# Kernel optimization log

Hardware: AMD Instinct MI355X
Metric: run time of the kernel (lower is better)

The kernel has to match this reference:

```python
import jax, jax.numpy as jnp
import numpy as np

HEADS, K = 8, 32
EPS = 1e-5


def bn(x, gamma, beta):
    # batch-stat BN over all axes except the last (channel) axis
    axes = tuple(range(x.ndim - 1))
    m = jnp.mean(x, axes, keepdims=True)
    v = jnp.var(x, axes, keepdims=True)
    return (x - m) / jnp.sqrt(v + EPS) * gamma + beta


def leaky(z):
    return jax.nn.leaky_relu(z, 0.2)


def conv1(t, W, g, b):  # 1x1 Conv1d + BN + LeakyReLU, channels-last
    return leaky(bn(jnp.einsum('bnc,dc->bnd', t, W), g, b))


def conv2(t, W, g, b):  # 1x1 Conv2d + BN + LeakyReLU on (B,N,k,C)
    return leaky(bn(jnp.einsum('bnkc,dc->bnkd', t, W), g, b))


def _forward(x, pos, Wq, gq, bq, Wk, gk, bk, Wv, gv, bv,
             Wpb, gpb, bpb, We1, ge1, be1, We2, ge2, be2,
             Wm1, gm1, bm1, Wm2, gm2, bm2):
    B, N, C = x.shape
    cph = C // HEADS
    q = conv1(x, Wq, gq, bq)
    key = conv1(x, Wk, gk, bk)
    val = conv1(x, Wv, gv, bv)
    # kNN in key-feature space (DGCNN-style get_graph_feature, edge_function='global')
    sq = jnp.sum(key * key, -1)                          # (B,N)
    dist = sq[:, :, None] + sq[:, None, :] - 2.0 * jnp.einsum('bnc,bmc->bnm', key, key)
    _, idx = jax.lax.top_k(-dist, K)                     # (B,N,K)
    bidx = jnp.arange(B)[:, None, None]
    key_nb = key[bidx, idx]                              # (B,N,K,C)
    val_nb = val[bidx, idx]
    pos_nb = pos[bidx, idx]
    mask = jnp.sign(idx + 1).astype(x.dtype)             # (B,N,K), all ones for valid knn
    masked_pos = (pos_nb - pos[:, :, None, :]) * mask[..., None]
    posb = conv2(masked_pos, Wpb, gpb, bpb)              # (B,N,K,C)
    vector = key_nb - q[:, :, None, :] + posb            # vector attention logits input
    value = val_nb + posb
    vector = conv2(conv2(vector, We1, ge1, be1), We2, ge2, be2)  # (B,N,K,cph)
    vector = jax.nn.softmax(vector, axis=2) * mask[..., None]    # softmax over k neighbors
    value = value.reshape(B, N, K, cph, HEADS)
    attn = jnp.einsum('bnkgh,bnkg->bngh', value, vector).reshape(B, N, C)
    x = x + attn
    h = jax.nn.silu(bn(jnp.einsum('bnc,dc->bnd', x, Wm1), gm1, bm1))
    m = jax.nn.silu(bn(jnp.einsum('bnc,dc->bnd', h, Wm2), gm2, bm2))
    return x + m


def setup_inputs():
    key = jax.random.key(0)
    ks = jax.random.split(key, 16)
    B, N, C, H = 2, 2048, 256, 512
    cph = C // HEADS
    s = 0.02
    inp = {
        'x': jax.random.normal(ks[0], (B, N, C), jnp.float32),
        'pos': jax.random.normal(ks[1], (B, N, C), jnp.float32),
        'Wq': jax.random.normal(ks[2], (C, C), jnp.float32) * s,
        'gq': jnp.ones((C,), jnp.float32), 'bq': jnp.zeros((C,), jnp.float32),
        'Wk': jax.random.normal(ks[3], (C, C), jnp.float32) * s,
        'gk': jnp.ones((C,), jnp.float32), 'bk': jnp.zeros((C,), jnp.float32),
        'Wv': jax.random.normal(ks[4], (C, C), jnp.float32) * s,
        'gv': jnp.ones((C,), jnp.float32), 'bv': jnp.zeros((C,), jnp.float32),
        'Wpb': jax.random.normal(ks[5], (C, C), jnp.float32) * s,
        'gpb': jnp.ones((C,), jnp.float32), 'bpb': jnp.zeros((C,), jnp.float32),
        'We1': jax.random.normal(ks[6], (cph, C), jnp.float32) * s,
        'ge1': jnp.ones((cph,), jnp.float32), 'be1': jnp.zeros((cph,), jnp.float32),
        'We2': jax.random.normal(ks[7], (cph, cph), jnp.float32) * s,
        'ge2': jnp.ones((cph,), jnp.float32), 'be2': jnp.zeros((cph,), jnp.float32),
        'Wm1': jax.random.normal(ks[8], (H, C), jnp.float32) * s,
        'gm1': jnp.ones((H,), jnp.float32), 'bm1': jnp.zeros((H,), jnp.float32),
        'Wm2': jax.random.normal(ks[9], (C, H), jnp.float32) * s,
        'gm2': jnp.ones((C,), jnp.float32), 'bm2': jnp.zeros((C,), jnp.float32),
    }
    return inp


def reference(x, pos, Wq, gq, bq, Wk, gk, bk, Wv, gv, bv,
              Wpb, gpb, bpb, We1, ge1, be1, We2, ge2, be2,
              Wm1, gm1, bm1, Wm2, gm2, bm2):
    return _forward(x, pos, Wq, gq, bq, Wk, gk, bk, Wv, gv, bv,
                    Wpb, gpb, bpb, We1, ge1, be1, We2, ge2, be2,
                    Wm1, gm1, bm1, Wm2, gm2, bm2)
```

## Files before the change

### kernel.cpp

```cpp
#include <hip/hip_runtime.h>

#define EPS 1e-5f

typedef __attribute__((ext_vector_type(8))) short s8v;
typedef __attribute__((ext_vector_type(4))) float f4v;

__device__ __forceinline__ float leakyf(float z){ return z >= 0.f ? z : 0.2f*z; }
__device__ __forceinline__ float siluf(float y){ return y / (1.f + __expf(-y)); }
__device__ __forceinline__ unsigned f2bfu(float f){
  unsigned u = __float_as_uint(f);
  return (u + 0x7FFFu + ((u>>16)&1u)) >> 16;
}
__device__ __forceinline__ unsigned short bfr(float f){ return (unsigned short)f2bfu(f); }
__device__ __forceinline__ float bf2f16(unsigned short s){ return __uint_as_float(((unsigned)s)<<16); }

__global__ __launch_bounds__(256) void k_zero(float* __restrict__ p, int n){
  int i = blockIdx.x*256 + threadIdx.x;
  if (i < n) p[i] = 0.f;
}

template<bool TRANSA, bool STATS, bool FULL4>
__global__ __launch_bounds__(256) void k_gemm(
    const float* __restrict__ A, int lda, long aStr,
    const float* __restrict__ A3, int lda3,
    const float* __restrict__ fAbuck, float invnA, int CA,
    const float* __restrict__ gA, const float* __restrict__ bA,
    const float* __restrict__ B0, const float* __restrict__ B1,
    const float* __restrict__ B2, const float* __restrict__ B3, int ldb, long bStr,
    float* __restrict__ C, int ldc, long cStr,
    float* __restrict__ C3, int ldc3,
    int K, float* __restrict__ buck, int statC, int statChanStr)
{
  __shared__ unsigned short Ah[2048], Al[2048], Bh[2048], Bl[2048];
  __shared__ float Ssum[STATS?64:4], Ssq[STATS?64:4];
  __shared__ float mrA[TRANSA?1024:4];
  const int z = blockIdx.z;
  const bool zAlt = (A3 != nullptr) && (z == 3);
  const float* Az = zAlt ? A3 : A + (long)z*aStr;
  const int ldaz = zAlt ? lda3 : lda;
  const float* Bb = (z==0?B0 : z==1?B1 : (z==2?B2:B3)) + (long)z*bStr;
  float* Cb = zAlt ? C3 : (C + (long)z*cStr);
  const int ldcz = zAlt ? ldc3 : ldc;
  const bool doStats = STATS && !zAlt;
  const int tid = threadIdx.x;
  const int bm = blockIdx.x*64, bn = blockIdx.y*64;
  const int wv = tid>>6, lane = tid&63;
  const int lm = lane&15, quad = lane>>4;
  if (doStats && tid<64){ Ssum[tid]=0.f; Ssq[tid]=0.f; }
  if (TRANSA){
    for (int c = tid; c < CA; c += 256){
      float s=0.f, q=0.f;
      for (int b=0;b<64;b++){ s += fAbuck[(long)b*2*CA + c]; q += fAbuck[(long)b*2*CA + CA + c]; }
      float m = s*invnA;
      float v = fmaxf(q*invnA - m*m, 0.f);
      mrA[c] = m; mrA[CA + c] = rsqrtf(v + EPS);
    }
    __syncthreads();
  }

  const int r0 = tid>>3, kg = tid&7;
  const int qk = kg>>1, j0 = (kg&1)*4;
  const int s0 = ((((r0>>4)  )*4 + qk)*16 + ((r0&15)^qk))*8 + j0;
  const int s1 = ((((r0>>4)+2)*4 + qk)*16 + ((r0&15)^qk))*8 + j0;
  const float* aP0 = Az + (long)(bm+r0)*ldaz + kg*4;
  const float* aP1 = aP0 + (long)32*ldaz;
  const float* bP0 = Bb + (long)(bn+r0)*ldb + kg*4;
  const float* bP1 = bP0 + (long)32*ldb;

  f4v acc[4];
  #pragma unroll
  for (int j=0;j<4;j++) acc[j] = (f4v){0.f,0.f,0.f,0.f};

  float4 a0 = *(const float4*)(aP0);
  float4 a1 = *(const float4*)(aP1);
  float4 b0 = *(const float4*)(bP0);
  float4 b1 = *(const float4*)(bP1);

  for (int k0=0; k0<K; k0+=32){
    float4 av0 = a0, av1 = a1;
    if (TRANSA){
      float4 m4 = *(const float4*)&mrA[k0 + kg*4];
      float4 r4 = *(const float4*)&mrA[CA + k0 + kg*4];
      float4 g4 = *(const float4*)(gA + k0 + kg*4);
      float4 b4 = *(const float4*)(bA + k0 + kg*4);
      av0.x = siluf((av0.x - m4.x)*r4.x*g4.x + b4.x);
      av0.y = siluf((av0.y - m4.y)*r4.y*g4.y + b4.y);
      av0.z = siluf((av0.z - m4.z)*r4.z*g4.z + b4.z);
      av0.w = siluf((av0.w - m4.w)*r4.w*g4.w + b4.w);
      av1.x = siluf((av1.x - m4.x)*r4.x*g4.x + b4.x);
      av1.y = siluf((av1.y - m4.y)*r4.y*g4.y + b4.y);
      av1.z = siluf((av1.z - m4.z)*r4.z*g4.z + b4.z);
      av1.w = siluf((av1.w - m4.w)*r4.w*g4.w + b4.w);
    }
    ushort4 h4, l4;
    h4.x=bfr(av0.x); l4.x=bfr(av0.x-bf2f16(h4.x));
    h4.y=bfr(av0.y); l4.y=bfr(av0.y-bf2f16(h4.y));
    h4.z=bfr(av0.z); l4.z=bfr(av0.z-bf2f16(h4.z));
    h4.w=bfr(av0.w); l4.w=bfr(av0.w-bf2f16(h4.w));
    *(ushort4*)&Ah[s0]=h4; *(ushort4*)&Al[s0]=l4;
    h4.x=bfr(av1.x); l4.x=bfr(av1.x-bf2f16(h4.x));
    h4.y=bfr(av1.y); l4.y=bfr(av1.y-bf2f16(h4.y));
    h4.z=bfr(av1.z); l4.z=bfr(av1.z-bf2f16(h4.z));
    h4.w=bfr(av1.w); l4.w=bfr(av1.w-bf2f16(h4.w));
    *(ushort4*)&Ah[s1]=h4; *(ushort4*)&Al[s1]=l4;
    h4.x=bfr(b0.x); l4.x=bfr(b0.x-bf2f16(h4.x));
    h4.y=bfr(b0.y); l4.y=bfr(b0.y-bf2f16(h4.y));
    h4.z=bfr(b0.z); l4.z=bfr(b0.z-bf2f16(h4.z));
    h4.w=bfr(b0.w); l4.w=bfr(b0.w-bf2f16(h4.w));
    *(ushort4*)&Bh[s0]=h4; *(ushort4*)&Bl[s0]=l4;
    h4.x=bfr(b1.x); l4.x=bfr(b1.x-bf2f16(h4.x));
    h4.y=bfr(b1.y); l4.y=bfr(b1.y-bf2f16(h4.y));
    h4.z=bfr(b1.z); l4.z=bfr(b1.z-bf2f16(h4.z));
    h4.w=bfr(b1.w); l4.w=bfr(b1.w-bf2f16(h4.w));
    *(ushort4*)&Bh[s1]=h4; *(ushort4*)&Bl[s1]=l4;
    __syncthreads();
    if (k0+32 < K){
      a0 = *(const float4*)(aP0 + k0+32);
      a1 = *(const float4*)(aP1 + k0+32);
      b0 = *(const float4*)(bP0 + k0+32);
      b1 = *(const float4*)(bP1 + k0+32);
    }
    const int soA = ((wv*4 + quad)*16 + (lm^quad))*8;
    s8v ah = *(const s8v*)&Ah[soA];
    s8v al = *(const s8v*)&Al[soA];
    #pragma unroll
    for (int j=0;j<4;j++){
      const int soB = ((j*4 + quad)*16 + (lm^quad))*8;
      s8v bh = *(const s8v*)&Bh[soB];
      s8v bl = *(const s8v*)&Bl[soB];
      acc[j] = __builtin_amdgcn_mfma_f32_16x16x32_bf16(ah, bh, acc[j], 0,0,0);
      acc[j] = __builtin_amdgcn_mfma_f32_16x16x32_bf16(ah, bl, acc[j], 0,0,0);
      acc[j] = __builtin_amdgcn_mfma_f32_16x16x32_bf16(al, bh, acc[j], 0,0,0);
      if (FULL4)
        acc[j] = __builtin_amdgcn_mfma_f32_16x16x32_bf16(al, bl, acc[j], 0,0,0);
    }
    __syncthreads();
  }
  #pragma unroll
  for (int rr=0;rr<4;rr++){
    float* cr = Cb + (long)(bm + wv*16 + quad*4 + rr)*ldcz + bn + lm;
    #pragma unroll
    for (int j=0;j<4;j++) cr[j*16] = acc[j][rr];
  }
  if (doStats){
    #pragma unroll
    for (int j=0;j<4;j++){
      float s=0.f, q=0.f;
      #pragma unroll
      for (int rr=0;rr<4;rr++){ float v = acc[j][rr]; s += v; q += v*v; }
      s += __shfl_xor(s,16,64); s += __shfl_xor(s,32,64);
      q += __shfl_xor(q,16,64); q += __shfl_xor(q,32,64);
      if (quad==0){ atomicAdd(&Ssum[j*16+lm], s); atomicAdd(&Ssq[j*16+lm], q); }
    }
    __syncthreads();
    if (tid < 64){
      int chan = statChanStr*z + bn + tid;
      float* bb = buck + (long)(blockIdx.x & 63)*2*statC;
      atomicAdd(&bb[chan], Ssum[tid]);
      atomicAdd(&bb[statC + chan], Ssq[tid]);
    }
  }
}

__global__ void k_finalize(const float* __restrict__ buck, int C, float invn, float* __restrict__ mr){
  int c = blockIdx.x*256 + threadIdx.x;
  if (c < C){
    float s=0,q=0;
    for (int b=0;b<64;b++){ s += buck[(long)b*2*C + c]; q += buck[(long)b*2*C + C + c]; }
    float m = s*invn;
    float v = fmaxf(q*invn - m*m, 0.f);
    mr[c] = m; mr[C+c] = rsqrtf(v + EPS);
  }
}

__global__ __launch_bounds__(256) void k_apply_qkv(const float* __restrict__ raw, const float* __restrict__ bQKV,
    const float* __restrict__ gq, const float* __restrict__ bq,
    const float* __restrict__ gk, const float* __restrict__ bk,
    const float* __restrict__ gv, const float* __restrict__ bv,
    float* __restrict__ key, float* __restrict__ qv, float* __restrict__ sq){
  __shared__ float mrs[1536];
  __shared__ float red[4];
  const int tid = threadIdx.x;
  const int wv = tid>>6, lane = tid&63;
  for (int c = tid; c < 768; c += 256){
    float s=0.f, q=0.f;
    for (int b=0;b<64;b++){ s += bQKV[(long)b*1536 + c]; q += bQKV[(long)b*1536 + 768 + c]; }
    float m = s*(1.f/4096.f);
    float v = fmaxf(q*(1.f/4096.f) - m*m, 0.f);
    mrs[c] = m; mrs[768+c] = rsqrtf(v + EPS);
  }
  __syncthreads();
  const float gqv = gq[tid], bqv = bq[tid], gkv = gk[tid], bkv = bk[tid], gvv = gv[tid], bvv = bv[tid];
  for (int rr=0; rr<8; rr++){
    const long r = (long)blockIdx.x*8 + rr;
    const float* row = raw + r*768;
    float zq = row[tid], zk = row[256+tid], zv = row[512+tid];
    float yq = leakyf((zq - mrs[tid])*mrs[768+tid]*gqv + bqv);
    float yk = leakyf((zk - mrs[256+tid])*mrs[1024+tid]*gkv + bkv);
    float yv = leakyf((zv - mrs[512+tid])*mrs[1280+tid]*gvv + bvv);
    qv[r*512 + tid] = yq;
    key[r*256 + tid] = yk;
    qv[r*512 + 256 + tid] = yv;
    float kq = yk*yk;
    kq += __shfl_xor(kq,1,64); kq += __shfl_xor(kq,2,64);
    kq += __shfl_xor(kq,4,64); kq += __shfl_xor(kq,8,64);
    kq += __shfl_xor(kq,16,64); kq += __shfl_xor(kq,32,64);
    if (lane==0) red[wv] = kq;
    __syncthreads();
    if (tid==0) sq[r] = red[0]+red[1]+red[2]+red[3];
    __syncthreads();
  }
}

__global__ __launch_bounds__(256) void k_topk(const float* __restrict__ G2, const float* __restrict__ sq,
    int* __restrict__ idxb, const float* __restrict__ P, float* __restrict__ bPB){
  __shared__ unsigned Ds[4][2048];
  __shared__ int Ws[4][32];
  const int wv = threadIdx.x >> 6, lane = threadIdx.x & 63;
  const int row = blockIdx.x*4 + wv;
  const int b = row >> 11, n = row & 2047;
  const float* Grow = G2 + (long)b*4194304 + (long)n*2048;
  const float* sqb = sq + b*2048;
  const float sqn = sqb[n];
  const unsigned long long SEN = 0xFFFFFFFFFFFFFFFFull;
  unsigned long long k0=SEN,k1=SEN,k2=SEN,k3=SEN;
  #pragma unroll
  for (int j=0;j<32;j++){
    int m = lane + j*64;
    float d = sqn + sqb[m] - 2.f*Grow[m];
    unsigned u = __float_as_uint(d);
    u ^= ((unsigned)((int)u >> 31)) | 0x80000000u;
    Ds[wv][m] = u;
    unsigned long long kk = ((unsigned long long)u << 32) | (unsigned)m;
    if (kk < k3){
      k3 = kk;
      if (k3 < k2){ unsigned long long t_=k2; k2=k3; k3=t_; }
      if (k2 < k1){ unsigned long long t_=k1; k1=k2; k2=t_; }
      if (k1 < k0){ unsigned long long t_=k0; k0=k1; k1=t_; }
    }
  }
  int* orow = idxb + row*32;
  for (int t=0;t<32;t++){
    unsigned long long v = k0;
    #pragma unroll
    for (int off=32; off; off>>=1){
      unsigned long long v2 = (unsigned long long)__shfl_xor((long long)v, off, 64);
      if (v2 < v) v = v2;
    }
    int wi = (int)(v & 0xFFFFFFFFull);
    if (lane == 0){ orow[t] = wi; Ws[wv][t] = wi; }
    if (v == k0){
      Ds[wv][wi] = 0xFFFFFFFFu;
      k0=k1; k1=k2; k2=k3; k3=SEN;
      if (k0 == SEN){
        for (int j=0;j<32;j++){
          int m = lane + j*64;
          unsigned u = Ds[wv][m];
          if (u != 0xFFFFFFFFu){
            unsigned long long kk = ((unsigned long long)u << 32) | (unsigned)m;
            if (kk < k3){
              k3 = kk;
              if (k3 < k2){ unsigned long long t_=k2; k2=k3; k3=t_; }
              if (k2 < k1){ unsigned long long t_=k1; k1=k2; k2=t_; }
              if (k1 < k0){ unsigned long long t_=k0; k0=k1; k1=t_; }
            }
          }
        }
      }
    }
  }
  const long bbase = (long)b << 11;
  const int c4 = lane*4;
  float4 pn = *(const float4*)(P + (long)row*256 + c4);
  float s0=0,s1=0,s2=0,s3=0,q0=0,q1=0,q2=0,q3=0;
  #pragma unroll
  for (int t=0;t<32;t++){
    float4 pg = *(const float4*)(P + (bbase + Ws[wv][t])*256 + c4);
    float z0 = pg.x - pn.x, z1 = pg.y - pn.y, z2 = pg.z - pn.z, z3 = pg.w - pn.w;
    s0+=z0; q0+=z0*z0; s1+=z1; q1+=z1*z1;
    s2+=z2; q2+=z2*z2; s3+=z3; q3+=z3*z3;
  }
  float* bb = bPB + (long)(blockIdx.x & 63)*512;
  atomicAdd(&bb[c4+0], s0); atomicAdd(&bb[c4+1], s1);
  atomicAdd(&bb[c4+2], s2); atomicAdd(&bb[c4+3], s3);
  atomicAdd(&bb[256+c4+0], q0); atomicAdd(&bb[256+c4+1], q1);
  atomicAdd(&bb[256+c4+2], q2); atomicAdd(&bb[256+c4+3], q3);
}

__global__ __launch_bounds__(256) void k_e1m(
    const float* __restrict__ key, const float* __restrict__ qv, const float* __restrict__ P,
    const int* __restrict__ idx, const float* __restrict__ mrPB,
    const float* __restrict__ gpb, const float* __restrict__ bpb,
    const float* __restrict__ We1, float* __restrict__ E1, float* __restrict__ buckE1)
{
  __shared__ unsigned short Ab[16384];
  __shared__ unsigned short Wb[8192];
  __shared__ float Ssum[32], Ssq[32];
  const int tid = threadIdx.x;
  const int wv = tid>>6, lane = tid&63;
  const int quad = lane>>4, lm = lane&15;
  const int bn0 = blockIdx.x*2;
  if (tid < 32){ Ssum[tid]=0.f; Ssq[tid]=0.f; }
  for (int e = tid; e < 8192; e += 256){
    int d = e >> 8, c = e & 255;
    int off = (((d>>4)*8 + (c>>5))*4 + ((c>>3)&3))*128 + (d&15)*8 + (c&7);
    Wb[off] = bfr(We1[e]);
  }
  {
    const int bn = bn0 + (wv>>1);
    const long base = (long)(bn >> 11) << 11;
    const int c4 = lane*4;
    float4 q4  = *(const float4*)(qv + (long)bn*512 + c4);
    float4 pn4 = *(const float4*)(P + (long)bn*256 + c4);
    float4 mp4 = *(const float4*)(mrPB + c4);
    float4 rp4 = *(const float4*)(mrPB + 256 + c4);
    float4 g4  = *(const float4*)(gpb + c4);
    float4 b4  = *(const float4*)(bpb + c4);
    const int ksc = c4>>5, quadc = (c4>>3)&3, jc = c4&7;
    for (int j = 0; j < 16; ++j){
      const int rloc = wv*16 + j;
      const int kk = rloc & 31;
      const int g = idx[bn*32 + kk];
      float4 kb = *(const float4*)(key + (base+g)*256 + c4);
      float4 pb = *(const float4*)(P + (base+g)*256 + c4);
      float o0 = kb.x - q4.x + leakyf((pb.x - pn4.x - mp4.x)*rp4.x*g4.x + b4.x);
      float o1 = kb.y - q4.y + leakyf((pb.y - pn4.y - mp4.y)*rp4.y*g4.y + b4.y);
      float o2 = kb.z - q4.z + leakyf((pb.z - pn4.z - mp4.z)*rp4.z*g4.z + b4.z);
      float o3 = kb.w - q4.w + leakyf((pb.w - pn4.w - mp4.w)*rp4.w*g4.w + b4.w);
      const int atile = rloc >> 4;
      const int slot = ((rloc & 15) ^ (ksc<<1) ^ quadc) & 15;
      const int off = ((atile*8 + ksc)*4 + quadc)*128 + slot*8 + jc;
      ushort4 u; u.x = bfr(o0); u.y = bfr(o1); u.z = bfr(o2); u.w = bfr(o3);
      *(ushort4*)&Ab[off] = u;
    }
  }
  __syncthreads();
  f4v acc0 = (f4v){0,0,0,0}, acc1 = (f4v){0,0,0,0};
  #pragma unroll
  for (int ks=0; ks<8; ks++){
    const int aslot = (lm ^ (ks<<1) ^ quad) & 15;
    s8v a  = *(const s8v*)&Ab[((wv*8 + ks)*4 + quad)*128 + aslot*8];
    s8v b0 = *(const s8v*)&Wb[((ks)*4 + quad)*128 + lm*8];
    s8v b1 = *(const s8v*)&Wb[((8 + ks)*4 + quad)*128 + lm*8];
    acc0 = __builtin_amdgcn_mfma_f32_16x16x32_bf16(a, b0, acc0, 0,0,0);
    acc1 = __builtin_amdgcn_mfma_f32_16x16x32_bf16(a, b1, acc1, 0,0,0);
  }
  {
    const int bn = bn0 + (wv>>1);
    const int mt = wv & 1;
    #pragma unroll
    for (int rr=0; rr<4; rr++){
      int krow = mt*16 + quad*4 + rr;
      float* o = E1 + ((long)bn*32 + krow)*32;
      o[lm]      = acc0[rr];
      o[16 + lm] = acc1[rr];
    }
  }
  float s0=0,q0=0,s1=0,q1=0;
  #pragma unroll
  for (int rr=0; rr<4; rr++){
    s0 += acc0[rr]; q0 += acc0[rr]*acc0[rr];
    s1 += acc1[rr]; q1 += acc1[rr]*acc1[rr];
  }
  s0 += __shfl_xor(s0,16,64); s0 += __shfl_xor(s0,32,64);
  q0 += __shfl_xor(q0,16,64); q0 += __shfl_xor(q0,32,64);
  s1 += __shfl_xor(s1,16,64); s1 += __shfl_xor(s1,32,64);
  q1 += __shfl_xor(q1,16,64); q1 += __shfl_xor(q1,32,64);
  if (quad == 0){
    atomicAdd(&Ssum[lm], s0);      atomicAdd(&Ssq[lm], q0);
    atomicAdd(&Ssum[16+lm], s1);   atomicAdd(&Ssq[16+lm], q1);
  }
  __syncthreads();
  if (tid < 32){
    float* bb = buckE1 + (long)(blockIdx.x & 63)*64;
    atomicAdd(&bb[tid], Ssum[tid]); atomicAdd(&bb[32+tid], Ssq[tid]);
  }
}

__global__ __launch_bounds__(256) void k_e2m(
    float* __restrict__ E, const float* __restrict__ bE1buck,
    const float* __restrict__ ge1, const float* __restrict__ be1,
    const float* __restrict__ We2, float* __restrict__ buckE2)
{
  __shared__ unsigned short Ab[8192];
  __shared__ unsigned short Wb[1024];
  __shared__ float Ssum[32], Ssq[32];
  __shared__ float mrE1s[64];
  const int tid = threadIdx.x;
  const int wv = tid>>6, lane = tid&63;
  const int quad = lane>>4, lm = lane&15;
  const long r0 = (long)blockIdx.x*256;
  if (tid < 32){
    Ssum[tid]=0.f; Ssq[tid]=0.f;
    float s=0.f, q=0.f;
    for (int b=0;b<64;b++){ s += bE1buck[b*64+tid]; q += bE1buck[b*64+32+tid]; }
    float m = s*(1.f/131072.f);
    float v = fmaxf(q*(1.f/131072.f) - m*m, 0.f);
    mrE1s[tid] = m; mrE1s[32+tid] = rsqrtf(v + EPS);
  }
  for (int e = tid; e < 1024; e += 256){
    int d = e>>5, c = e&31;
    int off = ((d>>4)*4 + ((c>>3)&3))*128 + (d&15)*8 + (c&7);
    Wb[off] = bfr(We2[e]);
  }
  __syncthreads();
  #pragma unroll
  for (int it=0; it<8; it++){
    int e = (tid + it*256)*4;
    int row = e>>5, c = e&31;
    float4 v = *(const float4*)(E + (r0 + row)*32 + c);
    float4 m4 = *(const float4*)&mrE1s[c];
    float4 r4 = *(const float4*)&mrE1s[32+c];
    float4 g4 = *(const float4*)(ge1 + c);
    float4 b4 = *(const float4*)(be1 + c);
    float o0 = leakyf((v.x - m4.x)*r4.x*g4.x + b4.x);
    float o1 = leakyf((v.y - m4.y)*r4.y*g4.y + b4.y);
    float o2 = leakyf((v.z - m4.z)*r4.z*g4.z + b4.z);
    float o3 = leakyf((v.w - m4.w)*r4.w*g4.w + b4.w);
    int quadc = (c>>3)&3, jc = c&7;
    int slot = ((row&15) ^ quadc) & 15;
    int off = ((row>>4)*4 + quadc)*128 + slot*8 + jc;
    ushort4 u; u.x=bfr(o0); u.y=bfr(o1); u.z=bfr(o2); u.w=bfr(o3);
    *(ushort4*)&Ab[off] = u;
  }
  __syncthreads();
  f4v acc0[4], acc1[4];
  #pragma unroll
  for (int i=0;i<4;i++){ acc0[i]=(f4v){0,0,0,0}; acc1[i]=(f4v){0,0,0,0}; }
  const int aslot = (lm ^ quad) & 15;
  s8v b0 = *(const s8v*)&Wb[(quad)*128 + lm*8];
  s8v b1 = *(const s8v*)&Wb[(4 + quad)*128 + lm*8];
  #pragma unroll
  for (int i=0;i<4;i++){
    const int atile = wv*4 + i;
    s8v a = *(const s8v*)&Ab[(atile*4 + quad)*128 + aslot*8];
    acc0[i] = __builtin_amdgcn_mfma_f32_16x16x32_bf16(a, b0, acc0[i], 0,0,0);
    acc1[i] = __builtin_amdgcn_mfma_f32_16x16x32_bf16(a, b1, acc1[i], 0,0,0);
  }
  __syncthreads();
  float s0=0,q0=0,s1=0,q1=0;
  #pragma unroll
  for (int i=0;i<4;i++){
    const int atile = wv*4 + i;
    #pragma unroll
    for (int rr=0; rr<4; rr++){
      long row = r0 + atile*16 + quad*4 + rr;
      float* o = E + row*32;
      o[lm]      = acc0[i][rr];
      o[16 + lm] = acc1[i][rr];
      s0 += acc0[i][rr]; q0 += acc0[i][rr]*acc0[i][rr];
      s1 += acc1[i][rr]; q1 += acc1[i][rr]*acc1[i][rr];
    }
  }
  s0 += __shfl_xor(s0,16,64); s0 += __shfl_xor(s0,32,64);
  q0 += __shfl_xor(q0,16,64); q0 += __shfl_xor(q0,32,64);
  s1 += __shfl_xor(s1,16,64); s1 += __shfl_xor(s1,32,64);
  q1 += __shfl_xor(q1,16,64); q1 += __shfl_xor(q1,32,64);
  if (quad == 0){
    atomicAdd(&Ssum[lm], s0);    atomicAdd(&Ssq[lm], q0);
    atomicAdd(&Ssum[16+lm], s1); atomicAdd(&Ssq[16+lm], q1);
  }
  __syncthreads();
  if (tid < 32){
    float* bb = buckE2 + (long)(blockIdx.x & 63)*64;
    atomicAdd(&bb[tid], Ssum[tid]); atomicAdd(&bb[32+tid], Ssq[tid]);
  }
}

__global__ __launch_bounds__(256) void k_attn(
    const float* __restrict__ E2, const float* __restrict__ bE2buck,
    const float* __restrict__ ge2, const float* __restrict__ be2,
    const float* __restrict__ qv, const float* __restrict__ P, const int* __restrict__ idx,
    const float* __restrict__ mrPB, const float* __restrict__ gpb, const float* __restrict__ bpb,
    const float* __restrict__ xin, float* __restrict__ x2)
{
  __shared__ float L[4][32][33];
  __shared__ float mrE2s[64];
  const int tid = threadIdx.x;
  const int wv = tid>>6, lane = tid&63;
  if (tid < 32){
    float s=0.f, q=0.f;
    for (int b=0;b<64;b++){ s += bE2buck[b*64+tid]; q += bE2buck[b*64+32+tid]; }
    float m = s*(1.f/131072.f);
    float v = fmaxf(q*(1.f/131072.f) - m*m, 0.f);
    mrE2s[tid] = m; mrE2s[32+tid] = rsqrtf(v + EPS);
  }
  __syncthreads();
  const int bn = blockIdx.x*4 + wv;
  const long base = (long)(bn >> 11) << 11;
  for (int qq=0; qq<4; qq++){
    int e = lane*16 + qq*4;
    int k = e >> 5, g0 = e & 31;
    float4 v  = *(const float4*)(E2 + (long)bn*1024 + e);
    float4 m4 = *(const float4*)&mrE2s[g0];
    float4 r4 = *(const float4*)&mrE2s[32+g0];
    float4 g4 = *(const float4*)(ge2 + g0);
    float4 b4 = *(const float4*)(be2 + g0);
    L[wv][k][g0+0] = leakyf((v.x - m4.x)*r4.x*g4.x + b4.x);
    L[wv][k][g0+1] = leakyf((v.y - m4.y)*r4.y*g4.y + b4.y);
    L[wv][k][g0+2] = leakyf((v.z - m4.z)*r4.z*g4.z + b4.z);
    L[wv][k][g0+3] = leakyf((v.w - m4.w)*r4.w*g4.w + b4.w);
  }
  __syncthreads();
  {
    const int g = lane & 31, h = lane >> 5;
    float mx = -3.4e38f;
    for (int j=0;j<16;j++) mx = fmaxf(mx, L[wv][h*16+j][g]);
    mx = fmaxf(mx, __shfl_xor(mx, 32, 64));
    float sm = 0.f, ev[16];
    for (int j=0;j<16;j++){ float e_ = __expf(L[wv][h*16+j][g] - mx); ev[j] = e_; sm += e_; }
    sm += __shfl_xor(sm, 32, 64);
    float inv = 1.f/sm;
    for (int j=0;j<16;j++) L[wv][h*16+j][g] = ev[j]*inv;
  }
  __syncthreads();
  const int c4 = lane*4, gg = lane >> 1;
  float4 pn4 = *(const float4*)(P + (long)bn*256 + c4);
  float4 mp4 = *(const float4*)(mrPB + c4);
  float4 rp4 = *(const float4*)(mrPB + 256 + c4);
  float4 g4 = *(const float4*)(gpb + c4);
  float4 b4 = *(const float4*)(bpb + c4);
  float accv[4] = {0,0,0,0};
  const int* ir = idx + bn*32;
  for (int k=0;k<32;k++){
    int gi = ir[k];
    float4 vv = *(const float4*)(qv + (long)(base+gi)*512 + 256 + c4);
    float4 pp = *(const float4*)(P + (base+gi)*256 + c4);
    float w = L[wv][k][gg];
    float zh0 = (pp.x - pn4.x - mp4.x)*rp4.x*g4.x + b4.x;
    float zh1 = (pp.y - pn4.y - mp4.y)*rp4.y*g4.y + b4.y;
    float zh2 = (pp.z - pn4.z - mp4.z)*rp4.z*g4.z + b4.z;
    float zh3 = (pp.w - pn4.w - mp4.w)*rp4.w*g4.w + b4.w;
    accv[0] = fmaf(vv.x + leakyf(zh0), w, accv[0]);
    accv[1] = fmaf(vv.y + leakyf(zh1), w, accv[1]);
    accv[2] = fmaf(vv.z + leakyf(zh2), w, accv[2]);
    accv[3] = fmaf(vv.w + leakyf(zh3), w, accv[3]);
  }
  float4 x4 = *(const float4*)(xin + (long)bn*256 + c4);
  float4 o;
  o.x = x4.x + accv[0]; o.y = x4.y + accv[1];
  o.z = x4.z + accv[2]; o.w = x4.w + accv[3];
  *(float4*)(x2 + (long)bn*256 + c4) = o;
}

__global__ __launch_bounds__(256) void k_final(const float* __restrict__ x2, const float* __restrict__ Zm2,
    const float* __restrict__ bM2buck, const float* __restrict__ gm, const float* __restrict__ bm,
    float* __restrict__ out){
  __shared__ float mrs[512];
  const int tid = threadIdx.x;
  {
    float s=0.f, q=0.f;
    for (int b=0;b<64;b++){ s += bM2buck[(long)b*512 + tid]; q += bM2buck[(long)b*512 + 256 + tid]; }
    float m = s*(1.f/4096.f);
    float v = fmaxf(q*(1.f/4096.f) - m*m, 0.f);
    mrs[tid] = m; mrs[256+tid] = rsqrtf(v + EPS);
  }
  __syncthreads();
  const float gmv = gm[tid], bmv = bm[tid];
  #pragma unroll
  for (int rr=0; rr<8; rr++){
    long r = (long)blockIdx.x*8 + rr;
    float z = Zm2[r*256 + tid];
    float y = (z - mrs[tid])*mrs[256+tid]*gmv + bmv;
    out[r*256 + tid] = x2[r*256 + tid] + siluf(y);
  }
}

extern "C" void kernel_launch(void* const* d_in, const int* in_sizes, int n_in,
                              void* d_out, int out_size, void* d_ws, size_t ws_size,
                              hipStream_t stream){
  (void)in_sizes; (void)n_in; (void)out_size; (void)ws_size;
  const float* x   = (const float*)d_in[0];
  const float* pos = (const float*)d_in[1];
  const float* Wq  = (const float*)d_in[2];
  const float* gq  = (const float*)d_in[3];
  const float* bq  = (const float*)d_in[4];
  const float* Wk  = (const float*)d_in[5];
  const float* gk  = (const float*)d_in[6];
  const float* bk  = (const float*)d_in[7];
  const float* Wv  = (const float*)d_in[8];
  const float* gv  = (const float*)d_in[9];
  const float* bv  = (const float*)d_in[10];
  const float* Wpb = (const float*)d_in[11];
  const float* gpb = (const float*)d_in[12];
  const float* bpb = (const float*)d_in[13];
  const float* We1 = (const float*)d_in[14];
  const float* ge1 = (const float*)d_in[15];
  const float* be1 = (const float*)d_in[16];
  const float* We2 = (const float*)d_in[17];
  const float* ge2 = (const float*)d_in[18];
  const float* be2 = (const float*)d_in[19];
  const float* Wm1 = (const float*)d_in[20];
  const float* gm1 = (const float*)d_in[21];
  const float* bm1 = (const float*)d_in[22];
  const float* Wm2 = (const float*)d_in[23];
  const float* gm2 = (const float*)d_in[24];
  const float* bm2 = (const float*)d_in[25];

  float* w     = (float*)d_ws;
  float* arena = w;
  float* key   = w + 4194304;
  float* P     = w + 5242880;
  float* x2    = w + 6291456;
  float* qv    = w + 7340032;
  float* sq    = w + 9437184;
  int*   idx   = (int*)(w + 9441280);
  float* buck  = w + 9572352;
  float* mr    = w + 9809920;
  float* G2    = w + 9813632;
  float* bQKV = buck;            float* bPB = buck + 98304;  float* bE1 = buck + 131072;
  float* bE2  = buck + 135168;   float* bM1 = buck + 139264; float* bM2 = buck + 204800;
  float* mrPB = mr + 1536;
  float* Zm1 = arena;
  float* Zm2 = arena + 2097152;

  k_zero<<<928,256,0,stream>>>(buck, 237568);
  k_gemm<false,true,true><<<dim3(64,4,4),256,0,stream>>>(
      x,256,0, pos,256, nullptr,0.f,0, nullptr,nullptr,
      Wq,Wk,Wv,Wpb,256,0, arena,768,256, P,256, 256, bQKV,768,256);
  k_apply_qkv<<<512,256,0,stream>>>(arena, bQKV, gq,bq,gk,bk,gv,bv, key, qv, sq);
  k_gemm<false,false,true><<<dim3(32,32,2),256,0,stream>>>(
      key,256,524288, nullptr,0, nullptr,0.f,0, nullptr,nullptr,
      key,key,key,nullptr,256,524288, G2,2048,4194304, nullptr,0, 256, nullptr,0,0);
  k_topk<<<1024,256,0,stream>>>(G2, sq, idx, P, bPB);
  k_finalize<<<1,256,0,stream>>>(bPB, 256, 1.f/131072.f, mrPB);
  k_e1m<<<2048,256,0,stream>>>(key, qv, P, idx, mrPB, gpb, bpb, We1, arena, bE1);
  k_e2m<<<512,256,0,stream>>>(arena, bE1, ge1, be1, We2, bE2);
  k_attn<<<1024,256,0,stream>>>(arena, bE2, ge2, be2, qv, P, idx, mrPB, gpb, bpb, x, x2);
  k_gemm<false,true,false><<<dim3(64,8,1),256,0,stream>>>(
      x2,256,0, nullptr,0, nullptr,0.f,0, nullptr,nullptr,
      Wm1,Wm1,Wm1,nullptr,256,0, Zm1,512,0, nullptr,0, 256, bM1,512,0);
  k_gemm<true,true,false><<<dim3(64,4,1),256,0,stream>>>(
      Zm1,512,0, nullptr,0, bM1,1.f/4096.f,512, gm1,bm1,
      Wm2,Wm2,Wm2,nullptr,512,0, Zm2,256,0, nullptr,0, 512, bM2,256,0);
  k_final<<<512,256,0,stream>>>(x2, Zm2, bM2, gm2, bm2, (float*)d_out);
}
```

Baseline: 344.2 us.

## Split each top-k row across two waves and merge partial lists

Each kNN row's 2048 distances are now split between two wavefronts, each selecting its own 32 smallest over 1024 candidates. The two sorted lists are then merged with a per-lane binary search. The grid doubles to 2048 blocks and the position-difference statistics loop is divided between the two waves. This halves the serial per-wave scan and selection work and raises parallelism, at the cost of an extra block barrier, a merge step and more blocks issuing atomics.

```diff
diff --git a/kernel.cpp b/kernel.cpp
--- a/kernel.cpp
+++ b/kernel.cpp
@@ -214,24 +214,27 @@
 
 __global__ __launch_bounds__(256) void k_topk(const float* __restrict__ G2, const float* __restrict__ sq,
     int* __restrict__ idxb, const float* __restrict__ P, float* __restrict__ bPB){
-  __shared__ unsigned Ds[4][2048];
-  __shared__ int Ws[4][32];
+  __shared__ unsigned Ds[4][1024];
+  __shared__ unsigned long long M[4][32];
+  __shared__ int Wfin[2][32];
   const int wv = threadIdx.x >> 6, lane = threadIdx.x & 63;
-  const int row = blockIdx.x*4 + wv;
+  const int gw = blockIdx.x*4 + wv;
+  const int row = gw >> 1, half = gw & 1;
   const int b = row >> 11, n = row & 2047;
-  const float* Grow = G2 + (long)b*4194304 + (long)n*2048;
-  const float* sqb = sq + b*2048;
-  const float sqn = sqb[n];
+  const float* Grow = G2 + (long)b*4194304 + (long)n*2048 + half*1024;
+  const float* sqh  = sq + (long)b*2048 + half*1024;
+  const float sqn = sq[(long)b*2048 + n];
+  const unsigned mbase = half*1024;
   const unsigned long long SEN = 0xFFFFFFFFFFFFFFFFull;
   unsigned long long k0=SEN,k1=SEN,k2=SEN,k3=SEN;
   #pragma unroll
-  for (int j=0;j<32;j++){
-    int m = lane + j*64;
-    float d = sqn + sqb[m] - 2.f*Grow[m];
+  for (int j=0;j<16;j++){
+    int ml = lane + j*64;
+    float d = sqn + sqh[ml] - 2.f*Grow[ml];
     unsigned u = __float_as_uint(d);
     u ^= ((unsigned)((int)u >> 31)) | 0x80000000u;
-    Ds[wv][m] = u;
-    unsigned long long kk = ((unsigned long long)u << 32) | (unsigned)m;
+    Ds[wv][ml] = u;
+    unsigned long long kk = ((unsigned long long)u << 32) | (mbase + ml);
     if (kk < k3){
       k3 = kk;
       if (k3 < k2){ unsigned long long t_=k2; k2=k3; k3=t_; }
@@ -239,7 +242,6 @@
       if (k1 < k0){ unsigned long long t_=k0; k0=k1; k1=t_; }
     }
   }
-  int* orow = idxb + row*32;
   for (int t=0;t<32;t++){
     unsigned long long v = k0;
     #pragma unroll
@@ -247,17 +249,17 @@
       unsigned long long v2 = (unsigned long long)__shfl_xor((long long)v, off, 64);
       if (v2 < v) v = v2;
     }
-    int wi = (int)(v & 0xFFFFFFFFull);
-    if (lane == 0){ orow[t] = wi; Ws[wv][t] = wi; }
+    if (lane == 0) M[wv][t] = v;
     if (v == k0){
-      Ds[wv][wi] = 0xFFFFFFFFu;
+      int wl = ((int)(v & 0xFFFFFFFFull)) & 1023;
+      Ds[wv][wl] = 0xFFFFFFFFu;
       k0=k1; k1=k2; k2=k3; k3=SEN;
       if (k0 == SEN){
-        for (int j=0;j<32;j++){
-          int m = lane + j*64;
-          unsigned u = Ds[wv][m];
+        for (int j=0;j<16;j++){
+          int ml = lane + j*64;
+          unsigned u = Ds[wv][ml];
           if (u != 0xFFFFFFFFu){
-            unsigned long long kk = ((unsigned long long)u << 32) | (unsigned)m;
+            unsigned long long kk = ((unsigned long long)u << 32) | (mbase + ml);
             if (kk < k3){
               k3 = kk;
               if (k3 < k2){ unsigned long long t_=k2; k2=k3; k3=t_; }
@@ -269,13 +271,34 @@
       }
     }
   }
+  __syncthreads();
+  if ((wv & 1) == 0){
+    const int rloc = wv >> 1;
+    const unsigned long long* A  = M[wv];
+    const unsigned long long* Bx = M[wv+1];
+    const int t = lane & 31;
+    const bool useA = lane < 32;
+    unsigned long long e = useA ? A[t] : Bx[t];
+    const unsigned long long* other = useA ? Bx : A;
+    int lo = 0, hi = 32;
+    while (lo < hi){ int mid = (lo+hi)>>1; if (other[mid] < e) lo = mid+1; else hi = mid; }
+    int pos = t + lo;
+    if (pos < 32){
+      int m = (int)(e & 0xFFFFFFFFull);
+      Wfin[rloc][pos] = m;
+      idxb[(long)(blockIdx.x*2 + rloc)*32 + pos] = m;
+    }
+  }
+  __syncthreads();
   const long bbase = (long)b << 11;
   const int c4 = lane*4;
   float4 pn = *(const float4*)(P + (long)row*256 + c4);
   float s0=0,s1=0,s2=0,s3=0,q0=0,q1=0,q2=0,q3=0;
-  #pragma unroll
-  for (int t=0;t<32;t++){
-    float4 pg = *(const float4*)(P + (bbase + Ws[wv][t])*256 + c4);
+  const int rloc = wv >> 1;
+  #pragma unroll
+  for (int t=0;t<16;t++){
+    int g = Wfin[rloc][half*16 + t];
+    float4 pg = *(const float4*)(P + (bbase + g)*256 + c4);
     float z0 = pg.x - pn.x, z1 = pg.y - pn.y, z2 = pg.z - pn.z, z3 = pg.w - pn.w;
     s0+=z0; q0+=z0*z0; s1+=z1; q1+=z1*z1;
     s2+=z2; q2+=z2*z2; s3+=z3; q3+=z3*z3;
@@ -622,7 +645,7 @@
   k_gemm<false,false,true><<<dim3(32,32,2),256,0,stream>>>(
       key,256,524288, nullptr,0, nullptr,0.f,0, nullptr,nullptr,
       key,key,key,nullptr,256,524288, G2,2048,4194304, nullptr,0, 256, nullptr,0,0);
-  k_topk<<<1024,256,0,stream>>>(G2, sq, idx, P, bPB);
+  k_topk<<<2048,256,0,stream>>>(G2, sq, idx, P, bPB);
   k_finalize<<<1,256,0,stream>>>(bPB, 256, 1.f/131072.f, mrPB);
   k_e1m<<<2048,256,0,stream>>>(key, qv, P, idx, mrPB, gpb, bpb, We1, arena, bE1);
   k_e2m<<<512,256,0,stream>>>(arena, bE1, ge1, be1, We2, bE2);
```

After: 377.5 us. 9.7% more time.
